# Kernel optimization log

Hardware: AMD Instinct MI355X
Metric: run time of the kernel (lower is better)

Reference implementation:

```python
import jax, jax.numpy as jnp
import numpy as np

B, T, H, V, NT, NH, DFF = 2, 512, 768, 51865, 3, 4, 2048
EPS = 1e-5


def setup_inputs() -> dict:
    key = jax.random.key(0)
    ks = jax.random.split(key, 24)
    s = 0.02
    d = {
        "encoder_hidden": jax.random.normal(ks[0], (B, T, H), jnp.float32),
        "teacher_tokens": jax.random.randint(ks[1], (B, T, NT), 0, V, jnp.int32),
        "start_token": jax.random.normal(ks[2], (1, H), jnp.float32),
        "emb": jax.random.normal(ks[3], (V, H), jnp.float32) * s,
        # self-attention (torch MultiheadAttention packed qkv in_proj)
        "sa_in_w": jax.random.normal(ks[4], (3 * H, H), jnp.float32) * s,
        "sa_in_b": jnp.zeros((3 * H,), jnp.float32),
        "sa_out_w": jax.random.normal(ks[5], (H, H), jnp.float32) * s,
        "sa_out_b": jnp.zeros((H,), jnp.float32),
        # cross-attention
        "ca_in_w": jax.random.normal(ks[6], (3 * H, H), jnp.float32) * s,
        "ca_in_b": jnp.zeros((3 * H,), jnp.float32),
        "ca_out_w": jax.random.normal(ks[7], (H, H), jnp.float32) * s,
        "ca_out_b": jnp.zeros((H,), jnp.float32),
        # FFN
        "lin1_w": jax.random.normal(ks[8], (DFF, H), jnp.float32) * s,
        "lin1_b": jnp.zeros((DFF,), jnp.float32),
        "lin2_w": jax.random.normal(ks[9], (H, DFF), jnp.float32) * s,
        "lin2_b": jnp.zeros((H,), jnp.float32),
        # layer norms (post-norm TransformerDecoderLayer)
        "ln1_g": jnp.ones((H,), jnp.float32), "ln1_b": jnp.zeros((H,), jnp.float32),
        "ln2_g": jnp.ones((H,), jnp.float32), "ln2_b": jnp.zeros((H,), jnp.float32),
        "ln3_g": jnp.ones((H,), jnp.float32), "ln3_b": jnp.zeros((H,), jnp.float32),
        # output vocab projection (bias=False)
        "proj_w": jax.random.normal(ks[10], (V, H), jnp.float32) * s,
    }
    return d


def _ln(x, g, b):
    m = jnp.mean(x, -1, keepdims=True)
    v = jnp.mean(jnp.square(x - m), -1, keepdims=True)
    return (x - m) * jax.lax.rsqrt(v + EPS) * g + b


def _mha(xq, xkv, in_w, in_b, out_w, out_b, mask=None):
    # xq: (N, Lq, H), xkv: (N, Lk, H). torch packed in_proj: [Wq; Wk; Wv].
    h = xq.shape[-1]
    wq, wk, wv = jnp.split(in_w, 3, axis=0)
    bq, bk, bv = jnp.split(in_b, 3, axis=0)
    hd = h // NH
    q = (xq @ wq.T + bq).reshape(*xq.shape[:-1], NH, hd)
    k = (xkv @ wk.T + bk).reshape(*xkv.shape[:-1], NH, hd)
    v = (xkv @ wv.T + bv).reshape(*xkv.shape[:-1], NH, hd)
    scores = jnp.einsum("nqhd,nkhd->nhqk", q, k) / jnp.sqrt(jnp.float32(hd)).astype(q.dtype)
    if mask is not None:
        scores = scores + mask  # (Lq,Lk) additive causal mask
    a = jax.nn.softmax(scores, axis=-1)
    o = jnp.einsum("nhqk,nkhd->nqhd", a, v).reshape(*xq.shape[:-1], h)
    return o @ out_w.T + out_b


def _forward(encoder_hidden, teacher_tokens, start_token, emb,
             sa_in_w, sa_in_b, sa_out_w, sa_out_b,
             ca_in_w, ca_in_b, ca_out_w, ca_out_b,
             lin1_w, lin1_b, lin2_w, lin2_b,
             ln1_g, ln1_b, ln2_g, ln2_b, ln3_g, ln3_b, proj_w):
    b, t, h = encoder_hidden.shape
    nt = teacher_tokens.shape[-1]
    n = b * t
    # With teacher forcing + causal mask, step-i logits == position-i output of a
    # single decoder pass over [start, emb(teacher[..., :nt-1])] with memory of length 1.
    tok_emb = jnp.take(emb, teacher_tokens[:, :, : nt - 1], axis=0)  # (B,T,NT-1,H)
    start = jnp.broadcast_to(start_token.reshape(1, 1, 1, h), (b, t, 1, h))
    tgt = jnp.concatenate([start, tok_emb], axis=2).reshape(n, nt, h)  # (N,NT,H)
    mem = encoder_hidden.reshape(n, 1, h)  # (N,1,H)
    causal = jnp.where(jnp.triu(jnp.ones((nt, nt), bool), 1), -jnp.inf, 0.0).astype(tgt.dtype)
    # post-norm TransformerDecoderLayer (dropout=identity at eval)
    x = tgt
    x = _ln(x + _mha(x, x, sa_in_w, sa_in_b, sa_out_w, sa_out_b, causal), ln1_g, ln1_b)
    x = _ln(x + _mha(x, mem, ca_in_w, ca_in_b, ca_out_w, ca_out_b), ln2_g, ln2_b)
    ff = jax.nn.relu(x @ lin1_w.T + lin1_b) @ lin2_w.T + lin2_b
    x = _ln(x + ff, ln3_g, ln3_b)
    logits = x @ proj_w.T  # (N,NT,V)
    return logits.reshape(b, t, nt, -1)


def reference(encoder_hidden, teacher_tokens, start_token, emb,
              sa_in_w, sa_in_b, sa_out_w, sa_out_b,
              ca_in_w, ca_in_b, ca_out_w, ca_out_b,
              lin1_w, lin1_b, lin2_w, lin2_b,
              ln1_g, ln1_b, ln2_g, ln2_b, ln3_g, ln3_b, proj_w):
    return _forward(encoder_hidden, teacher_tokens, start_token, emb,
                    sa_in_w, sa_in_b, sa_out_w, sa_out_b,
                    ca_in_w, ca_in_b, ca_out_w, ca_out_b,
                    lin1_w, lin1_b, lin2_w, lin2_b,
                    ln1_g, ln1_b, ln2_g, ln2_b, ln3_g, ln3_b, proj_w)
```

## Files before the change

kernel.cpp:

```cpp
#include <hip/hip_runtime.h>

typedef __bf16 bf16;
typedef __bf16 bf16x4 __attribute__((ext_vector_type(4)));
typedef __bf16 bf16x8 __attribute__((ext_vector_type(8)));
typedef float f32x4 __attribute__((ext_vector_type(4)));

#define BM 128
#define BN 128
#define BK 32

__device__ __forceinline__ void async16(const void* g, void* l) {
    __builtin_amdgcn_global_load_lds(
        (__attribute__((address_space(1))) void*)g,
        (__attribute__((address_space(3))) void*)l,
        16, 0, 0);
}

__global__ __launch_bounds__(512, 2) void gemm256(
    const bf16* __restrict__ A, const bf16* __restrict__ W,
    float* __restrict__ C, int K, int ldo, int Nstore, int nTilesM)
{
    __shared__ bf16 lds[3][16384];

    int nwg = gridDim.x;
    int orig = blockIdx.x;
    int q = nwg >> 3, r = nwg & 7, xcd = orig & 7, local = orig >> 3;
    int wgid = (xcd < r ? xcd * (q + 1) : r * (q + 1) + (xcd - r) * q) + local;
    const int brow = (wgid % nTilesM) * 256;
    const int bcol = (wgid / nTilesM) * 256;

    const int t = threadIdx.x;
    const int wid = t >> 6, lane = t & 63;
    const int wm = wid >> 2, wn = wid & 3;
    const int l15 = lane & 15, lhi = lane >> 4;

    const int lr = t >> 2;
    const int ck = (t & 3) * 8;
    const bf16* srcA0 = A + (size_t)(brow + lr) * K + ck;
    const bf16* srcA1 = srcA0 + (size_t)128 * K;
    const int colB0 = ((lr >> 5) & 3) * 64 + (lr & 31);
    const bf16* srcB0 = W + (size_t)(bcol + colB0) * K + ck;
    const bf16* srcB1 = W + (size_t)(bcol + colB0 + 32) * K + ck;
    const int dstoff = wid * 512;

    const int aoff = (wm * 128 + l15) * 32 + lhi * 8;
    const int boff = (wn * 32 + l15) * 32 + lhi * 8 + 8192;

    f32x4 acc[8][4] = {};
    const int nkt = K >> 5;

    #pragma unroll
    for (int p = 0; p < 2; p++) {
        bf16* bb = &lds[p][0];
        const int k0 = p * 32;
        async16(srcA0 + k0, bb + dstoff);
        async16(srcA1 + k0, bb + 4096 + dstoff);
        async16(srcB0 + k0, bb + 8192 + dstoff);
        async16(srcB1 + k0, bb + 12288 + dstoff);
    }

    int cur = 0, stg = 2;
    for (int tt = 0; tt < nkt; ++tt) {
        const bf16* bufc = &lds[cur][0];
        bf16* bufs = &lds[stg][0];
        const int k2 = (tt + 2) << 5;
        const bool st = (tt < nkt - 2);

        if (tt < nkt - 1) asm volatile("s_waitcnt vmcnt(4)" ::: "memory");
        else              asm volatile("s_waitcnt vmcnt(0)" ::: "memory");
        __builtin_amdgcn_s_barrier();
        __builtin_amdgcn_sched_barrier(0);
        if (st) {
            async16(srcA0 + k2, bufs + dstoff);
            async16(srcA1 + k2, bufs + 4096 + dstoff);
        }
        bf16x8 a[4], b[4];
        #pragma unroll
        for (int j = 0; j < 4; j++)
            b[j] = *(const bf16x8*)(bufc + boff + (j >> 1) * 4096 + (j & 1) * 512);
        #pragma unroll
        for (int fi = 0; fi < 4; fi++)
            a[fi] = *(const bf16x8*)(bufc + aoff + fi * 512);
        __builtin_amdgcn_s_setprio(1);
        #pragma unroll
        for (int fi = 0; fi < 4; fi++)
            #pragma unroll
            for (int j = 0; j < 4; j++)
                acc[fi][j] = __builtin_amdgcn_mfma_f32_16x16x32_bf16(
                    a[fi], b[j], acc[fi][j], 0, 0, 0);
        __builtin_amdgcn_s_setprio(0);

        if (st) {
            async16(srcB0 + k2, bufs + 8192 + dstoff);
            async16(srcB1 + k2, bufs + 12288 + dstoff);
        }
        __builtin_amdgcn_s_barrier();
        __builtin_amdgcn_sched_barrier(0);
        #pragma unroll
        for (int fi = 0; fi < 4; fi++)
            a[fi] = *(const bf16x8*)(bufc + aoff + 2048 + fi * 512);
        __builtin_amdgcn_s_setprio(1);
        #pragma unroll
        for (int fi = 0; fi < 4; fi++)
            #pragma unroll
            for (int j = 0; j < 4; j++)
                acc[4 + fi][j] = __builtin_amdgcn_mfma_f32_16x16x32_bf16(
                    a[fi], b[j], acc[4 + fi][j], 0, 0, 0);
        __builtin_amdgcn_s_setprio(0);

        cur = (cur + 1 == 3) ? 0 : cur + 1;
        stg = (stg + 1 == 3) ? 0 : stg + 1;
    }

    float* ldsf = (float*)&lds[0][0];
    const int lhi4 = lhi * 4;
    #pragma unroll
    for (int qq = 0; qq < 4; qq++) {
        __syncthreads();
        if (wm == (qq >> 1)) {
            const int fbase = (qq & 1) * 4;
            #pragma unroll
            for (int fi4 = 0; fi4 < 4; fi4++) {
                #pragma unroll
                for (int fj = 0; fj < 4; fj++) {
                    f32x4 v = acc[fbase + fi4][fj];
                    int lrow0 = fi4 * 16 + lhi4;
                    int col = wn * 64 + fj * 16 + l15;
                    #pragma unroll
                    for (int r2 = 0; r2 < 4; r2++) {
                        int lrow = lrow0 + r2;
                        ldsf[lrow * 256 + (col ^ ((lrow & 12) << 1))] = v[r2];
                    }
                }
            }
        }
        __syncthreads();
        #pragma unroll
        for (int i = 0; i < 8; i++) {
            int c = i * 512 + t;
            int lrow = c >> 6, ch = c & 63;
            f32x4 v = *(const f32x4*)(ldsf + lrow * 256
                                      + ((ch ^ ((lrow & 12) >> 1)) * 4));
            int grow = brow + qq * 64 + lrow;
            int gcol = bcol + ch * 4;
            float* dst = C + (size_t)grow * ldo + gcol;
            if (gcol + 4 <= Nstore) {
                *(f32x4*)dst = v;
            } else {
                #pragma unroll
                for (int k2 = 0; k2 < 4; k2++)
                    if (gcol + k2 < Nstore) dst[k2] = v[k2];
            }
        }
    }
}

__global__ __launch_bounds__(256) void gemm_bt(
    const bf16* __restrict__ A, const bf16* __restrict__ W,
    const float* __restrict__ bias,
    float* __restrict__ outF, bf16* __restrict__ outB,
    int M, int K, int ldo, int Nstore, int relu)
{
    __shared__ bf16 As[BM * BK];
    __shared__ bf16 Ws[BN * BK];
    const int brow = blockIdx.y * BM;
    const int bcol = blockIdx.x * BN;
    const int t = threadIdx.x;
    const int wv = t >> 6;
    const int lane = t & 63;
    const int wrow = (wv >> 1) * 64;
    const int wcol = (wv & 1) * 64;

    f32x4 acc[4][4] = {};

    const int row0 = t >> 2;
    const int cg = (t & 3) * 8;
    const bf16* gA = A + (size_t)(brow + row0) * K + cg;
    const bf16* gW = W + (size_t)(bcol + row0) * K + cg;
    const size_t rstep = (size_t)64 * K;
    bf16* lA0 = As + wv * 512;
    bf16* lA1 = As + 2048 + wv * 512;
    bf16* lW0 = Ws + wv * 512;
    bf16* lW1 = Ws + 2048 + wv * 512;

    const int lrow = lane & 15;
    const int kg = (lane >> 4) * 8;

    for (int k0 = 0; k0 < K; k0 += BK) {
        if (k0) __syncthreads();
        async16(gA + k0, lA0);
        async16(gA + rstep + k0, lA1);
        async16(gW + k0, lW0);
        async16(gW + rstep + k0, lW1);
        __syncthreads();
        bf16x8 af[4], wf[4];
        #pragma unroll
        for (int i = 0; i < 4; i++)
            af[i] = *(const bf16x8*)(As + (wrow + i * 16 + lrow) * BK + kg);
        #pragma unroll
        for (int j = 0; j < 4; j++)
            wf[j] = *(const bf16x8*)(Ws + (wcol + j * 16 + lrow) * BK + kg);
        #pragma unroll
        for (int i = 0; i < 4; i++)
            #pragma unroll
            for (int j = 0; j < 4; j++)
                acc[i][j] = __builtin_amdgcn_mfma_f32_16x16x32_bf16(
                    af[i], wf[j], acc[i][j], 0, 0, 0);
    }

    const int lcol = lane & 15;
    const int rb = (lane >> 4) * 4;
    #pragma unroll
    for (int j = 0; j < 4; j++) {
        int n = bcol + wcol + j * 16 + lcol;
        if (n >= Nstore) continue;
        float bv = bias ? bias[n] : 0.f;
        #pragma unroll
        for (int i = 0; i < 4; i++) {
            #pragma unroll
            for (int r = 0; r < 4; r++) {
                int m = brow + wrow + i * 16 + rb + r;
                float v = acc[i][j][r] + bv;
                if (relu) v = fmaxf(v, 0.f);
                size_t off = (size_t)m * ldo + n;
                if (outF) outF[off] = v;
                if (outB) outB[off] = (bf16)v;
            }
        }
    }
}

__global__ __launch_bounds__(256) void cvt_bf16(
    const float* __restrict__ in, bf16* __restrict__ out,
    size_t nvalid, size_t ntotal)
{
    size_t i = ((size_t)blockIdx.x * 256 + threadIdx.x) * 4;
    if (i >= ntotal) return;
    bf16x4 r;
    if (i < nvalid) {
        f32x4 f = __builtin_nontemporal_load((const f32x4*)(in + i));
        r[0] = (bf16)f[0]; r[1] = (bf16)f[1]; r[2] = (bf16)f[2]; r[3] = (bf16)f[3];
    } else {
        r[0] = (bf16)0.f; r[1] = (bf16)0.f; r[2] = (bf16)0.f; r[3] = (bf16)0.f;
    }
    *(bf16x4*)(out + i) = r;
}

__global__ __launch_bounds__(256) void build_tgt(
    const float* __restrict__ start, const float* __restrict__ emb,
    const int* __restrict__ toks, float* __restrict__ outF, bf16* __restrict__ outB)
{
    int r = blockIdx.x;
    int n = r / 3, p = r % 3;
    const float* src = (p == 0) ? start : emb + (size_t)toks[n * 3 + (p - 1)] * 768;
    int t = threadIdx.x;
    #pragma unroll
    for (int j = 0; j < 3; j++) {
        int c = t + j * 256;
        float v = src[c];
        outF[(size_t)r * 768 + c] = v;
        outB[(size_t)r * 768 + c] = (bf16)v;
    }
}

__global__ __launch_bounds__(64) void attn3(
    const float* __restrict__ qkv, bf16* __restrict__ o)
{
    int blk = blockIdx.x;
    int n = blk >> 2, h = blk & 3;
    int lane = threadIdx.x;
    const float* base = qkv + (size_t)n * 3 * 2304 + h * 192;
    float q[3][3], k[3][3], v[3][3];
    #pragma unroll
    for (int p = 0; p < 3; p++)
        #pragma unroll
        for (int j = 0; j < 3; j++) {
            int d = lane + j * 64;
            q[p][j] = base[p * 2304 + d];
            k[p][j] = base[p * 2304 + 768 + d];
            v[p][j] = base[p * 2304 + 1536 + d];
        }
    float s[3][3];
    #pragma unroll
    for (int p = 0; p < 3; p++)
        #pragma unroll
        for (int pk = 0; pk < 3; pk++) {
            if (pk > p) continue;
            float ps = q[p][0] * k[pk][0] + q[p][1] * k[pk][1] + q[p][2] * k[pk][2];
            #pragma unroll
            for (int off = 32; off; off >>= 1) ps += __shfl_xor(ps, off);
            s[p][pk] = ps * 0.072168783648703220563f;
        }
    float a[3][3] = {};
    a[0][0] = 1.f;
    {
        float m = fmaxf(s[1][0], s[1][1]);
        float e0 = expf(s[1][0] - m), e1 = expf(s[1][1] - m);
        float inv = 1.f / (e0 + e1);
        a[1][0] = e0 * inv; a[1][1] = e1 * inv;
    }
    {
        float m = fmaxf(fmaxf(s[2][0], s[2][1]), s[2][2]);
        float e0 = expf(s[2][0] - m), e1 = expf(s[2][1] - m), e2 = expf(s[2][2] - m);
        float inv = 1.f / (e0 + e1 + e2);
        a[2][0] = e0 * inv; a[2][1] = e1 * inv; a[2][2] = e2 * inv;
    }
    bf16* ob = o + (size_t)n * 3 * 768 + h * 192;
    #pragma unroll
    for (int p = 0; p < 3; p++)
        #pragma unroll
        for (int j = 0; j < 3; j++) {
            float val = a[p][0] * v[0][j];
            if (p >= 1) val += a[p][1] * v[1][j];
            if (p >= 2) val += a[p][2] * v[2][j];
            ob[p * 768 + lane + j * 64] = (bf16)val;
        }
}

__global__ __launch_bounds__(256) void add_ln(
    const float* __restrict__ a, const float* __restrict__ b,
    const float* __restrict__ g, const float* __restrict__ be,
    float* __restrict__ outF, bf16* __restrict__ outB, int bcast)
{
    int r = blockIdx.x;
    int t = threadIdx.x;
    const float* ar = a + (size_t)r * 768;
    const float* br = b + (size_t)(bcast ? (r / 3) : r) * 768;
    float x[3];
    float s = 0.f, sq = 0.f;
    #pragma unroll
    for (int j = 0; j < 3; j++) {
        int c = t + j * 256;
        x[j] = ar[c] + br[c];
        s += x[j]; sq += x[j] * x[j];
    }
    #pragma unroll
    for (int off = 32; off; off >>= 1) {
        s += __shfl_xor(s, off);
        sq += __shfl_xor(sq, off);
    }
    __shared__ float ls[4], lq[4];
    int wv = t >> 6;
    if ((t & 63) == 0) { ls[wv] = s; lq[wv] = sq; }
    __syncthreads();
    s = ls[0] + ls[1] + ls[2] + ls[3];
    sq = lq[0] + lq[1] + lq[2] + lq[3];
    float mean = s * (1.f / 768.f);
    float var = sq * (1.f / 768.f) - mean * mean;
    float inv = rsqrtf(var + 1e-5f);
    #pragma unroll
    for (int j = 0; j < 3; j++) {
        int c = t + j * 256;
        float y = (x[j] - mean) * inv * g[c] + be[c];
        if (outF) outF[(size_t)r * 768 + c] = y;
        if (outB) outB[(size_t)r * 768 + c] = (bf16)y;
    }
}

static inline void run_gemm(const bf16* A, const bf16* W, const float* bias,
                            float* outF, bf16* outB, int M, int Npad, int K,
                            int ldo, int Nstore, int relu, hipStream_t s)
{
    dim3 grid(Npad / BN, M / BM);
    gemm_bt<<<grid, 256, 0, s>>>(A, W, bias, outF, outB, M, K, ldo, Nstore, relu);
}

static inline void run_cvt(const float* in, bf16* out, size_t nvalid,
                           size_t ntotal, hipStream_t s)
{
    int blocks = (int)((ntotal / 4 + 255) / 256);
    cvt_bf16<<<blocks, 256, 0, s>>>(in, out, nvalid, ntotal);
}

extern "C" void kernel_launch(void* const* d_in, const int* in_sizes, int n_in,
                              void* d_out, int out_size, void* d_ws, size_t ws_size,
                              hipStream_t stream)
{
    const float* enc      = (const float*)d_in[0];
    const int*   toks     = (const int*)d_in[1];
    const float* start    = (const float*)d_in[2];
    const float* emb      = (const float*)d_in[3];
    const float* sa_in_w  = (const float*)d_in[4];
    const float* sa_in_b  = (const float*)d_in[5];
    const float* sa_out_w = (const float*)d_in[6];
    const float* sa_out_b = (const float*)d_in[7];
    const float* ca_in_w  = (const float*)d_in[8];
    const float* ca_in_b  = (const float*)d_in[9];
    const float* ca_out_w = (const float*)d_in[10];
    const float* ca_out_b = (const float*)d_in[11];
    const float* lin1_w   = (const float*)d_in[12];
    const float* lin1_b   = (const float*)d_in[13];
    const float* lin2_w   = (const float*)d_in[14];
    const float* lin2_b   = (const float*)d_in[15];
    const float* ln1_g    = (const float*)d_in[16];
    const float* ln1_bb   = (const float*)d_in[17];
    const float* ln2_g    = (const float*)d_in[18];
    const float* ln2_bb   = (const float*)d_in[19];
    const float* ln3_g    = (const float*)d_in[20];
    const float* ln3_bb   = (const float*)d_in[21];
    const float* proj_w   = (const float*)d_in[22];
    float* out = (float*)d_out;

    const int NTOK = 3072;
    const int NM   = 1024;
    const int H    = 768;
    const int V    = 51865;
    const int VPAD = 51968;
    const int DFF  = 2048;

    char* p = (char*)d_ws;
    auto alloc = [&](size_t bytes) {
        void* r = (void*)p;
        p += (bytes + 255) & ~(size_t)255;
        return r;
    };
    float* tgt_f = (float*)alloc((size_t)NTOK * H * 4);
    float* x1_f  = (float*)alloc((size_t)NTOK * H * 4);
    float* x2_f  = (float*)alloc((size_t)NTOK * H * 4);
    float* big_f = (float*)alloc((size_t)NTOK * 2304 * 4);
    bf16*  actA  = (bf16*)alloc((size_t)NTOK * 2304 * 2);
    bf16*  actB  = (bf16*)alloc((size_t)NTOK * DFF * 2);
    bf16*  Wbf   = (bf16*)alloc((size_t)VPAD * H * 2);
    bf16*  mem_bf = actB;
    bf16*  v_bf   = actB + (size_t)NM * H;
    float* cao_f  = big_f + (size_t)NTOK * H;

    build_tgt<<<NTOK, 256, 0, stream>>>(start, emb, toks, tgt_f, actA);

    run_cvt(sa_in_w, Wbf, (size_t)2304 * H, (size_t)2304 * H, stream);
    run_gemm(actA, Wbf, sa_in_b, big_f, nullptr, NTOK, 2304, H, 2304, 2304, 0, stream);

    attn3<<<NM * 4, 64, 0, stream>>>(big_f, actA);

    run_cvt(sa_out_w, Wbf, (size_t)H * H, (size_t)H * H, stream);
    run_gemm(actA, Wbf, sa_out_b, big_f, nullptr, NTOK, H, H, H, H, 0, stream);

    add_ln<<<NTOK, 256, 0, stream>>>(tgt_f, big_f, ln1_g, ln1_bb, x1_f, nullptr, 0);

    run_cvt(enc, mem_bf, (size_t)NM * H, (size_t)NM * H, stream);
    run_cvt(ca_in_w + (size_t)1536 * H, Wbf, (size_t)H * H, (size_t)H * H, stream);
    run_gemm(mem_bf, Wbf, ca_in_b + 1536, nullptr, v_bf, NM, H, H, H, H, 0, stream);
    run_cvt(ca_out_w, Wbf, (size_t)H * H, (size_t)H * H, stream);
    run_gemm(v_bf, Wbf, ca_out_b, cao_f, nullptr, NM, H, H, H, H, 0, stream);

    add_ln<<<NTOK, 256, 0, stream>>>(x1_f, cao_f, ln2_g, ln2_bb, x2_f, actA, 1);

    run_cvt(lin1_w, Wbf, (size_t)DFF * H, (size_t)DFF * H, stream);
    run_gemm(actA, Wbf, lin1_b, nullptr, actB, NTOK, DFF, H, DFF, DFF, 1, stream);

    run_cvt(lin2_w, Wbf, (size_t)H * DFF, (size_t)H * DFF, stream);
    run_gemm(actB, Wbf, lin2_b, big_f, nullptr, NTOK, H, DFF, H, H, 0, stream);

    add_ln<<<NTOK, 256, 0, stream>>>(x2_f, big_f, ln3_g, ln3_bb, nullptr, actA, 0);

    run_cvt(proj_w, Wbf, (size_t)V * H, (size_t)VPAD * H, stream);
    {
        dim3 grid((NTOK / 256) * (VPAD / 256));
        gemm256<<<grid, 512, 0, stream>>>(actA, Wbf, out, H, V, V, NTOK / 256);
    }
}
```

Before: 637.0 us.

## Restructure vocab GEMM to BK=64 double-buffered pipeline with swizzled LDS and nontemporal stores

Measured after the change: 549.2 us. -13.8%, faster.

```diff
diff --git a/kernel.cpp b/kernel.cpp
--- a/kernel.cpp
+++ b/kernel.cpp
@@ -16,11 +16,11 @@
         16, 0, 0);
 }
 
-__global__ __launch_bounds__(512, 2) void gemm256(
+__global__ __launch_bounds__(512, 2) void gemm8p(
     const bf16* __restrict__ A, const bf16* __restrict__ W,
     float* __restrict__ C, int K, int ldo, int Nstore, int nTilesM)
 {
-    __shared__ bf16 lds[3][16384];
+    __shared__ bf16 lds[2][32768];
 
     int nwg = gridDim.x;
     int orig = blockIdx.x;
@@ -32,120 +32,147 @@
     const int t = threadIdx.x;
     const int wid = t >> 6, lane = t & 63;
     const int wm = wid >> 2, wn = wid & 3;
-    const int l15 = lane & 15, lhi = lane >> 4;
-
-    const int lr = t >> 2;
-    const int ck = (t & 3) * 8;
-    const bf16* srcA0 = A + (size_t)(brow + lr) * K + ck;
-    const bf16* srcA1 = srcA0 + (size_t)128 * K;
-    const int colB0 = ((lr >> 5) & 3) * 64 + (lr & 31);
-    const bf16* srcB0 = W + (size_t)(bcol + colB0) * K + ck;
-    const bf16* srcB1 = W + (size_t)(bcol + colB0 + 32) * K + ck;
-    const int dstoff = wid * 512;
-
-    const int aoff = (wm * 128 + l15) * 32 + lhi * 8;
-    const int boff = (wn * 32 + l15) * 32 + lhi * 8 + 8192;
+    const int l15 = lane & 15, l7 = lane & 7, lhi = lane >> 4;
+
+    const int lr = t >> 3;
+    const int cc = (t & 7) ^ (lr & 7);
+    const bf16* gA = A + (size_t)(brow + lr) * K + cc * 8;
+    const bf16* gW = W + (size_t)(bcol + lr) * K + cc * 8;
+    const int dsto = wid * 512;
+
+    const int kx0 = ((0 * 4 + lhi) ^ l7) * 8;
+    const int kx1 = ((1 * 4 + lhi) ^ l7) * 8;
+    const int abase = wm * 8192 + l15 * 64;
+    const int bbase = 16384 + (wn >> 1) * 8192 + ((wn & 1) * 64 + l15) * 64;
 
     f32x4 acc[8][4] = {};
-    const int nkt = K >> 5;
-
-    #pragma unroll
-    for (int p = 0; p < 2; p++) {
-        bf16* bb = &lds[p][0];
-        const int k0 = p * 32;
-        async16(srcA0 + k0, bb + dstoff);
-        async16(srcA1 + k0, bb + 4096 + dstoff);
-        async16(srcB0 + k0, bb + 8192 + dstoff);
-        async16(srcB1 + k0, bb + 12288 + dstoff);
-    }
-
-    int cur = 0, stg = 2;
-    for (int tt = 0; tt < nkt; ++tt) {
-        const bf16* bufc = &lds[cur][0];
-        bf16* bufs = &lds[stg][0];
-        const int k2 = (tt + 2) << 5;
-        const bool st = (tt < nkt - 2);
-
-        if (tt < nkt - 1) asm volatile("s_waitcnt vmcnt(4)" ::: "memory");
-        else              asm volatile("s_waitcnt vmcnt(0)" ::: "memory");
+    const int nkt = K >> 6;
+
+    #define ST_A(dst, k0)                                             \
+        async16(gA + (k0),                   (dst) + dsto);           \
+        async16(gA + (size_t)64 * K + (k0),  (dst) + 4096 + dsto);    \
+        async16(gA + (size_t)128 * K + (k0), (dst) + 8192 + dsto);    \
+        async16(gA + (size_t)192 * K + (k0), (dst) + 12288 + dsto);
+    #define ST_B(dst, k0)                                                     \
+        async16(gW + (k0),                   (dst) + 16384 + dsto);           \
+        async16(gW + (size_t)64 * K + (k0),  (dst) + 20480 + dsto);           \
+        async16(gW + (size_t)128 * K + (k0), (dst) + 24576 + dsto);           \
+        async16(gW + (size_t)192 * K + (k0), (dst) + 28672 + dsto);
+
+    { ST_A(&lds[0][0], 0); ST_B(&lds[0][0], 0); }
+
+    bf16x8 a[4][2], b[4][2];
+    for (int kt = 0; kt < nkt; ++kt) {
+        const bf16* cur = &lds[kt & 1][0];
+        bf16* stg = &lds[(kt + 1) & 1][0];
+        const int k1 = (kt + 1) << 6;
+        const bool st = (kt + 1 < nkt);
+
+        if (st) { ST_A(stg, k1); }
+        if (st) asm volatile("s_waitcnt vmcnt(4)" ::: "memory");
+        else    asm volatile("s_waitcnt vmcnt(0)" ::: "memory");
         __builtin_amdgcn_s_barrier();
-        __builtin_amdgcn_sched_barrier(0);
-        if (st) {
-            async16(srcA0 + k2, bufs + dstoff);
-            async16(srcA1 + k2, bufs + 4096 + dstoff);
-        }
-        bf16x8 a[4], b[4];
-        #pragma unroll
-        for (int j = 0; j < 4; j++)
-            b[j] = *(const bf16x8*)(bufc + boff + (j >> 1) * 4096 + (j & 1) * 512);
+        #pragma unroll
+        for (int fi = 0; fi < 4; fi++) {
+            a[fi][0] = *(const bf16x8*)(cur + abase + fi * 1024 + kx0);
+            a[fi][1] = *(const bf16x8*)(cur + abase + fi * 1024 + kx1);
+        }
+        #pragma unroll
+        for (int fj = 0; fj < 4; fj++) {
+            b[fj][0] = *(const bf16x8*)(cur + bbase + fj * 1024 + kx0);
+            b[fj][1] = *(const bf16x8*)(cur + bbase + fj * 1024 + kx1);
+        }
+        __builtin_amdgcn_s_setprio(1);
         #pragma unroll
         for (int fi = 0; fi < 4; fi++)
-            a[fi] = *(const bf16x8*)(bufc + aoff + fi * 512);
+            #pragma unroll
+            for (int fj = 0; fj < 2; fj++) {
+                f32x4 c0 = acc[fi][fj];
+                c0 = __builtin_amdgcn_mfma_f32_16x16x32_bf16(a[fi][0], b[fj][0], c0, 0,0,0);
+                c0 = __builtin_amdgcn_mfma_f32_16x16x32_bf16(a[fi][1], b[fj][1], c0, 0,0,0);
+                acc[fi][fj] = c0;
+            }
+        __builtin_amdgcn_s_setprio(0);
+        __builtin_amdgcn_s_barrier();
+
+        if (st) { ST_B(stg, k1); }
         __builtin_amdgcn_s_setprio(1);
         #pragma unroll
         for (int fi = 0; fi < 4; fi++)
             #pragma unroll
-            for (int j = 0; j < 4; j++)
-                acc[fi][j] = __builtin_amdgcn_mfma_f32_16x16x32_bf16(
-                    a[fi], b[j], acc[fi][j], 0, 0, 0);
+            for (int fj = 2; fj < 4; fj++) {
+                f32x4 c0 = acc[fi][fj];
+                c0 = __builtin_amdgcn_mfma_f32_16x16x32_bf16(a[fi][0], b[fj][0], c0, 0,0,0);
+                c0 = __builtin_amdgcn_mfma_f32_16x16x32_bf16(a[fi][1], b[fj][1], c0, 0,0,0);
+                acc[fi][fj] = c0;
+            }
         __builtin_amdgcn_s_setprio(0);
-
-        if (st) {
-            async16(srcB0 + k2, bufs + 8192 + dstoff);
-            async16(srcB1 + k2, bufs + 12288 + dstoff);
-        }
         __builtin_amdgcn_s_barrier();
-        __builtin_amdgcn_sched_barrier(0);
+
+        #pragma unroll
+        for (int fi = 0; fi < 4; fi++) {
+            a[fi][0] = *(const bf16x8*)(cur + abase + 4096 + fi * 1024 + kx0);
+            a[fi][1] = *(const bf16x8*)(cur + abase + 4096 + fi * 1024 + kx1);
+        }
+        __builtin_amdgcn_s_setprio(1);
         #pragma unroll
         for (int fi = 0; fi < 4; fi++)
-            a[fi] = *(const bf16x8*)(bufc + aoff + 2048 + fi * 512);
+            #pragma unroll
+            for (int fj = 0; fj < 2; fj++) {
+                f32x4 c0 = acc[4 + fi][fj];
+                c0 = __builtin_amdgcn_mfma_f32_16x16x32_bf16(a[fi][0], b[fj][0], c0, 0,0,0);
+                c0 = __builtin_amdgcn_mfma_f32_16x16x32_bf16(a[fi][1], b[fj][1], c0, 0,0,0);
+                acc[4 + fi][fj] = c0;
+            }
+        __builtin_amdgcn_s_setprio(0);
+        __builtin_amdgcn_s_barrier();
+
         __builtin_amdgcn_s_setprio(1);
         #pragma unroll
         for (int fi = 0; fi < 4; fi++)
             #pragma unroll
-            for (int j = 0; j < 4; j++)
-                acc[4 + fi][j] = __builtin_amdgcn_mfma_f32_16x16x32_bf16(
-                    a[fi], b[j], acc[4 + fi][j], 0, 0, 0);
+            for (int fj = 2; fj < 4; fj++) {
+                f32x4 c0 = acc[4 + fi][fj];
+                c0 = __builtin_amdgcn_mfma_f32_16x16x32_bf16(a[fi][0], b[fj][0], c0, 0,0,0);
+                c0 = __builtin_amdgcn_mfma_f32_16x16x32_bf16(a[fi][1], b[fj][1], c0, 0,0,0);
+                acc[4 + fi][fj] = c0;
+            }
         __builtin_amdgcn_s_setprio(0);
-
-        cur = (cur + 1 == 3) ? 0 : cur + 1;
-        stg = (stg + 1 == 3) ? 0 : stg + 1;
-    }
+    }
+    #undef ST_A
+    #undef ST_B
 
     float* ldsf = (float*)&lds[0][0];
     const int lhi4 = lhi * 4;
     #pragma unroll
-    for (int qq = 0; qq < 4; qq++) {
-        __syncthreads();
-        if (wm == (qq >> 1)) {
-            const int fbase = (qq & 1) * 4;
-            #pragma unroll
-            for (int fi4 = 0; fi4 < 4; fi4++) {
+    for (int h = 0; h < 2; h++) {
+        if (h) __builtin_amdgcn_s_barrier();
+        #pragma unroll
+        for (int fi4 = 0; fi4 < 4; fi4++) {
+            #pragma unroll
+            for (int fj = 0; fj < 4; fj++) {
+                f32x4 v = acc[h * 4 + fi4][fj];
+                int row0 = wm * 64 + fi4 * 16 + lhi4;
+                int col = wn * 64 + fj * 16 + l15;
                 #pragma unroll
-                for (int fj = 0; fj < 4; fj++) {
-                    f32x4 v = acc[fbase + fi4][fj];
-                    int lrow0 = fi4 * 16 + lhi4;
-                    int col = wn * 64 + fj * 16 + l15;
-                    #pragma unroll
-                    for (int r2 = 0; r2 < 4; r2++) {
-                        int lrow = lrow0 + r2;
-                        ldsf[lrow * 256 + (col ^ ((lrow & 12) << 1))] = v[r2];
-                    }
+                for (int r2 = 0; r2 < 4; r2++) {
+                    int row = row0 + r2;
+                    ldsf[row * 256 + (col ^ ((row & 12) << 1))] = v[r2];
                 }
             }
         }
-        __syncthreads();
-        #pragma unroll
-        for (int i = 0; i < 8; i++) {
+        __builtin_amdgcn_s_barrier();
+        #pragma unroll
+        for (int i = 0; i < 16; i++) {
             int c = i * 512 + t;
-            int lrow = c >> 6, ch = c & 63;
-            f32x4 v = *(const f32x4*)(ldsf + lrow * 256
-                                      + ((ch ^ ((lrow & 12) >> 1)) * 4));
-            int grow = brow + qq * 64 + lrow;
+            int row = c >> 6, ch = c & 63;
+            f32x4 v = *(const f32x4*)(ldsf + row * 256
+                                      + ((ch ^ ((row & 12) >> 1)) << 2));
+            int grow = brow + (row >> 6) * 128 + h * 64 + (row & 63);
             int gcol = bcol + ch * 4;
             float* dst = C + (size_t)grow * ldo + gcol;
             if (gcol + 4 <= Nstore) {
-                *(f32x4*)dst = v;
+                __builtin_nontemporal_store(v, (f32x4*)dst);
             } else {
                 #pragma unroll
                 for (int k2 = 0; k2 < 4; k2++)
@@ -456,6 +483,6 @@
     run_cvt(proj_w, Wbf, (size_t)V * H, (size_t)VPAD * H, stream);
     {
         dim3 grid((NTOK / 256) * (VPAD / 256));
-        gemm256<<<grid, 512, 0, stream>>>(actA, Wbf, out, H, V, V, NTOK / 256);
-    }
-}
+        gemm8p<<<grid, 512, 0, stream>>>(actA, Wbf, out, H, V, V, NTOK / 256);
+    }
+}
```
